# Kernel tuning notes

Hardware: AMD Instinct MI355X
Metric: run time of the kernel (lower is better)

The kernel has to match this reference:

```python
import jax, jax.numpy as jnp
import numpy as np

HEAD_DIM = 128
ALPHA0 = 1.0 / np.sqrt(HEAD_DIM).astype(np.float32)
ALPHA1 = 1.0


def setup_inputs() -> dict:
    key = jax.random.key(0)
    kq, kk, kv, kb = jax.random.split(key, 4)
    B, H, S, D = 2, 12, 2048, HEAD_DIM
    return {
        "q": jax.random.normal(kq, (B, H, S, D), dtype=jnp.float32),
        "k": jax.random.normal(kk, (B, H, S, D), dtype=jnp.float32),
        "v": jax.random.normal(kv, (B, H, S, D), dtype=jnp.float32),
        "bias": jax.random.normal(kb, (B, H, S, S), dtype=jnp.float32),
    }


def reference(q, k, v, bias):
    # output = alpha1 * sigmoid(alpha0 * (Q @ K^T) + bias) @ V
    scores = jnp.einsum("bhsd,bhtd->bhst", q, k)  # [B,H,S,S]
    attn = ALPHA1 * jax.nn.sigmoid(ALPHA0 * scores + bias)
    return jnp.einsum("bhst,bhtd->bhsd", attn, v)  # [B,H,S,D]
```

## Files before the change

### kernel.cpp

```cpp
#include <hip/hip_runtime.h>

typedef __attribute__((ext_vector_type(4))) float f32x4;
typedef __attribute__((ext_vector_type(8))) short short8v;
typedef __attribute__((ext_vector_type(2))) unsigned int uint2v;
typedef __attribute__((ext_vector_type(4))) unsigned int uint4v;

static constexpr int Sdim = 2048;
static constexpr int Ddim = 128;
static constexpr int BN   = 64;
static constexpr float kAlpha0 = 0.08838834764831844f;

__device__ __forceinline__ unsigned int bfpack(float a, float b) {
  unsigned int ua = __builtin_bit_cast(unsigned int, a);
  unsigned int ub = __builtin_bit_cast(unsigned int, b);
  ua = (ua + 0x7FFFu + ((ua >> 16) & 1u)) >> 16;
  ub = (ub + 0x7FFFu + ((ub >> 16) & 1u)) >> 16;
  return (ua & 0xFFFFu) | (ub << 16);
}

__device__ __forceinline__ float fast_sigmoid(float x) {
  return __builtin_amdgcn_rcpf(1.0f + __expf(-x));
}

__global__ __launch_bounds__(256, 2) void sigattn_kernel(
    const float* __restrict__ Q, const float* __restrict__ K,
    const float* __restrict__ V, const float* __restrict__ Bias,
    float* __restrict__ Out) {
  __shared__ __align__(16) unsigned char ldsK[BN * 256];
  __shared__ __align__(16) unsigned char ldsV[Ddim * 128];

  const int b    = blockIdx.x;
  const int xcd  = b & 7;
  const int jj   = b >> 3;
  const int head = xcd * 3 + (jj >> 4);
  const int q0   = (jj & 15) * 128;

  const int tid   = threadIdx.x;
  const int w     = tid >> 6;
  const int lane  = tid & 63;
  const int g     = lane >> 4;
  const int qlane = lane & 15;

  const float* __restrict__ Qh = Q + (size_t)head * Sdim * Ddim;
  const float* __restrict__ Kh = K + (size_t)head * Sdim * Ddim;
  const float* __restrict__ Vh = V + (size_t)head * Sdim * Ddim;
  const float* __restrict__ Bh = Bias + (size_t)head * Sdim * Sdim;
  float* __restrict__ Oh = Out + (size_t)head * Sdim * Ddim;

  short8v qfrag[2][4];
#pragma unroll
  for (int nf = 0; nf < 2; ++nf) {
    const float* qp = Qh + (size_t)(q0 + w * 32 + nf * 16 + qlane) * Ddim;
#pragma unroll
    for (int kf = 0; kf < 4; ++kf) {
      const int d0 = kf * 32 + g * 8;
      f32x4 a = *(const f32x4*)(qp + d0);
      f32x4 c = *(const f32x4*)(qp + d0 + 4);
      uint4v u;
      u[0] = bfpack(a[0], a[1]);
      u[1] = bfpack(a[2], a[3]);
      u[2] = bfpack(c[0], c[1]);
      u[3] = bfpack(c[2], c[3]);
      qfrag[nf][kf] = __builtin_bit_cast(short8v, u);
    }
  }

  const f32x4 fzero = {0.0f, 0.0f, 0.0f, 0.0f};
  f32x4 oacc[2][8];
#pragma unroll
  for (int qf = 0; qf < 2; ++qf)
#pragma unroll
    for (int nd = 0; nd < 8; ++nd) oacc[qf][nd] = fzero;

  const int idxA = ((((2 * g) & 3) * 16 + qlane) << 2);
  const int idxB = ((((2 * g + 1) & 3) * 16 + qlane) << 2);
  const bool lowhalf = (lane < 32);

  for (int t = 0; t < Sdim / BN; ++t) {
    const int kv0 = t * BN;

    {
      const int rb = tid >> 5;
      const int c4 = (tid & 31) * 4;
#pragma unroll
      for (int p = 0; p < 8; ++p) {
        const int r = p * 8 + rb;
        f32x4 kk = *(const f32x4*)(Kh + (size_t)(kv0 + r) * Ddim + c4);
        uint2v u;
        u[0] = bfpack(kk[0], kk[1]);
        u[1] = bfpack(kk[2], kk[3]);
        *(uint2v*)(ldsK + r * 256 + ((c4 * 2) ^ ((r & 7) << 4))) = u;
      }
    }
#pragma unroll
    for (int hh = 0; hh < 2; ++hh) {
      const int vb = tid + hh * 256;
      const int r0 = (vb >> 5) * 4;
      const int d4 = (vb & 31) * 4;
      f32x4 v0 = *(const f32x4*)(Vh + (size_t)(kv0 + r0 + 0) * Ddim + d4);
      f32x4 v1 = *(const f32x4*)(Vh + (size_t)(kv0 + r0 + 1) * Ddim + d4);
      f32x4 v2 = *(const f32x4*)(Vh + (size_t)(kv0 + r0 + 2) * Ddim + d4);
      f32x4 v3 = *(const f32x4*)(Vh + (size_t)(kv0 + r0 + 3) * Ddim + d4);
#pragma unroll
      for (int dd = 0; dd < 4; ++dd) {
        const int d = d4 + dd;
        uint2v u;
        u[0] = bfpack(v0[dd], v1[dd]);
        u[1] = bfpack(v2[dd], v3[dd]);
        *(uint2v*)(ldsV + d * 128 + ((r0 * 2) ^ (((d ^ (d >> 2)) & 7) << 4))) = u;
      }
    }
    __syncthreads();

    f32x4 bb[4][2];
#pragma unroll
    for (int mf = 0; mf < 4; ++mf)
#pragma unroll
      for (int nf = 0; nf < 2; ++nf) {
        const int row = q0 + w * 32 + nf * 16 + qlane;
        const int col = kv0 + mf * 16 + g * 4;
        bb[mf][nf] = *(const f32x4*)(Bh + (size_t)row * Sdim + col);
      }

    f32x4 sacc[4][2];
#pragma unroll
    for (int mf = 0; mf < 4; ++mf)
#pragma unroll
      for (int nf = 0; nf < 2; ++nf) sacc[mf][nf] = fzero;
#pragma unroll
    for (int kf = 0; kf < 4; ++kf)
#pragma unroll
      for (int mf = 0; mf < 4; ++mf) {
        const int kv = mf * 16 + qlane;
        const int d0 = kf * 32 + g * 8;
        short8v kf8 = *(const short8v*)(ldsK + kv * 256 + ((d0 * 2) ^ ((kv & 7) << 4)));
#pragma unroll
        for (int nf = 0; nf < 2; ++nf)
          sacc[mf][nf] = __builtin_amdgcn_mfma_f32_16x16x32_bf16(
              kf8, qfrag[nf][kf], sacc[mf][nf], 0, 0, 0);
      }

    unsigned int pw[4][2][2];
#pragma unroll
    for (int mf = 0; mf < 4; ++mf)
#pragma unroll
      for (int nf = 0; nf < 2; ++nf) {
        float p0 = fast_sigmoid(sacc[mf][nf][0] * kAlpha0 + bb[mf][nf][0]);
        float p1 = fast_sigmoid(sacc[mf][nf][1] * kAlpha0 + bb[mf][nf][1]);
        float p2 = fast_sigmoid(sacc[mf][nf][2] * kAlpha0 + bb[mf][nf][2]);
        float p3 = fast_sigmoid(sacc[mf][nf][3] * kAlpha0 + bb[mf][nf][3]);
        pw[mf][nf][0] = bfpack(p0, p1);
        pw[mf][nf][1] = bfpack(p2, p3);
      }

    short8v pa[2][2];
#pragma unroll
    for (int nf = 0; nf < 2; ++nf)
#pragma unroll
      for (int a = 0; a < 2; ++a) {
        uint4v u;
        int lo, hi;
        lo = __builtin_amdgcn_ds_bpermute(idxA, (int)pw[2 * a][nf][0]);
        hi = __builtin_amdgcn_ds_bpermute(idxA, (int)pw[2 * a + 1][nf][0]);
        u[0] = (unsigned)(lowhalf ? lo : hi);
        lo = __builtin_amdgcn_ds_bpermute(idxA, (int)pw[2 * a][nf][1]);
        hi = __builtin_amdgcn_ds_bpermute(idxA, (int)pw[2 * a + 1][nf][1]);
        u[1] = (unsigned)(lowhalf ? lo : hi);
        lo = __builtin_amdgcn_ds_bpermute(idxB, (int)pw[2 * a][nf][0]);
        hi = __builtin_amdgcn_ds_bpermute(idxB, (int)pw[2 * a + 1][nf][0]);
        u[2] = (unsigned)(lowhalf ? lo : hi);
        lo = __builtin_amdgcn_ds_bpermute(idxB, (int)pw[2 * a][nf][1]);
        hi = __builtin_amdgcn_ds_bpermute(idxB, (int)pw[2 * a + 1][nf][1]);
        u[3] = (unsigned)(lowhalf ? lo : hi);
        pa[nf][a] = __builtin_bit_cast(short8v, u);
      }

#pragma unroll
    for (int a = 0; a < 2; ++a)
#pragma unroll
      for (int nd = 0; nd < 8; ++nd) {
        const int d = nd * 16 + qlane;
        const int kvr = a * 32 + g * 8;
        short8v vf = *(const short8v*)(ldsV + d * 128 + ((kvr * 2) ^ (((d ^ (d >> 2)) & 7) << 4)));
#pragma unroll
        for (int qf = 0; qf < 2; ++qf)
          oacc[qf][nd] = __builtin_amdgcn_mfma_f32_16x16x32_bf16(
              pa[qf][a], vf, oacc[qf][nd], 0, 0, 0);
      }
    __syncthreads();
  }

#pragma unroll
  for (int qf = 0; qf < 2; ++qf)
#pragma unroll
    for (int nd = 0; nd < 8; ++nd) {
#pragma unroll
      for (int r = 0; r < 4; ++r) {
        const int row = q0 + w * 32 + qf * 16 + g * 4 + r;
        Oh[(size_t)row * Ddim + nd * 16 + qlane] = oacc[qf][nd][r];
      }
    }
}

extern "C" void kernel_launch(void* const* d_in, const int* in_sizes, int n_in,
                              void* d_out, int out_size, void* d_ws, size_t ws_size,
                              hipStream_t stream) {
  (void)in_sizes; (void)n_in; (void)d_ws; (void)ws_size; (void)out_size;
  const float* q    = (const float*)d_in[0];
  const float* k    = (const float*)d_in[1];
  const float* v    = (const float*)d_in[2];
  const float* bias = (const float*)d_in[3];
  float* out = (float*)d_out;
  dim3 grid(384), block(256);
  hipLaunchKernelGGL(sigattn_kernel, grid, block, 0, stream, q, k, v, bias, out);
}
```

Baseline: 632.3 us.

## Precompute bf16 K and transposed V, prefetch tiles via direct-to-LDS loads

```diff
diff --git a/kernel.cpp b/kernel.cpp
--- a/kernel.cpp
+++ b/kernel.cpp
@@ -2,12 +2,12 @@
 
 typedef __attribute__((ext_vector_type(4))) float f32x4;
 typedef __attribute__((ext_vector_type(8))) short short8v;
-typedef __attribute__((ext_vector_type(2))) unsigned int uint2v;
 typedef __attribute__((ext_vector_type(4))) unsigned int uint4v;
 
 static constexpr int Sdim = 2048;
 static constexpr int Ddim = 128;
 static constexpr int BN   = 64;
+static constexpr int NT   = Sdim / BN;
 static constexpr float kAlpha0 = 0.08838834764831844f;
 
 __device__ __forceinline__ unsigned int bfpack(float a, float b) {
@@ -17,23 +17,78 @@
   ub = (ub + 0x7FFFu + ((ub >> 16) & 1u)) >> 16;
   return (ua & 0xFFFFu) | (ub << 16);
 }
-
+__device__ __forceinline__ unsigned short bf1(float a) {
+  unsigned int ua = __builtin_bit_cast(unsigned int, a);
+  return (unsigned short)((ua + 0x7FFFu + ((ua >> 16) & 1u)) >> 16);
+}
 __device__ __forceinline__ float fast_sigmoid(float x) {
   return __builtin_amdgcn_rcpf(1.0f + __expf(-x));
 }
-
-__global__ __launch_bounds__(256, 2) void sigattn_kernel(
-    const float* __restrict__ Q, const float* __restrict__ K,
-    const float* __restrict__ V, const float* __restrict__ Bias,
+__device__ __forceinline__ void gll16(const void* g, void* l) {
+  __builtin_amdgcn_global_load_lds(
+      (const __attribute__((address_space(1))) unsigned int*)g,
+      (__attribute__((address_space(3))) unsigned int*)l, 16, 0, 0);
+}
+
+__global__ __launch_bounds__(256) void prep_kernel(
+    const float* __restrict__ K, const float* __restrict__ V,
+    unsigned short* __restrict__ Kb, unsigned short* __restrict__ Vt) {
+  __shared__ unsigned short ldsT[128 * 128];
+  const int head = blockIdx.x >> 4;
+  const int tile = blockIdx.x & 15;
+  const int t = threadIdx.x;
+  const float* Kh = K + ((size_t)head * Sdim + tile * 128) * Ddim;
+  const float* Vh = V + ((size_t)head * Sdim + tile * 128) * Ddim;
+  unsigned short* Kbh = Kb + ((size_t)head * Sdim + tile * 128) * Ddim;
+  unsigned short* Vth = Vt + (size_t)head * Ddim * Sdim + tile * 128;
+
+#pragma unroll
+  for (int c = 0; c < 8; ++c) {
+    const int e8 = c * 256 + t;
+    f32x4 a = *(const f32x4*)(Kh + e8 * 8);
+    f32x4 b = *(const f32x4*)(Kh + e8 * 8 + 4);
+    uint4v u;
+    u[0] = bfpack(a[0], a[1]); u[1] = bfpack(a[2], a[3]);
+    u[2] = bfpack(b[0], b[1]); u[3] = bfpack(b[2], b[3]);
+    *(uint4v*)(Kbh + e8 * 8) = u;
+  }
+#pragma unroll
+  for (int c = 0; c < 16; ++c) {
+    const int e4 = c * 256 + t;
+    const int kv = e4 >> 5;
+    const int c4 = (e4 & 31) * 4;
+    f32x4 v = *(const f32x4*)(Vh + (size_t)kv * Ddim + c4);
+#pragma unroll
+    for (int j = 0; j < 4; ++j) {
+      const int d = c4 + j;
+      const int sw = (d >> 2) & 7;
+      ldsT[d * 128 + ((((kv >> 3) ^ sw) << 3) | (kv & 7))] = bf1(v[j]);
+    }
+  }
+  __syncthreads();
+#pragma unroll
+  for (int c = 0; c < 8; ++c) {
+    const int G = c * 256 + t;
+    const int d = G >> 4;
+    const int s = G & 15;
+    const int sw = (d >> 2) & 7;
+    uint4v u = *(const uint4v*)(ldsT + d * 128 + ((s ^ sw) << 3));
+    *(uint4v*)(Vth + (size_t)d * Sdim + s * 8) = u;
+  }
+}
+
+__global__ __launch_bounds__(128, 2) void sigattn_kernel(
+    const float* __restrict__ Q, const unsigned short* __restrict__ Kb,
+    const unsigned short* __restrict__ Vt, const float* __restrict__ Bias,
     float* __restrict__ Out) {
-  __shared__ __align__(16) unsigned char ldsK[BN * 256];
-  __shared__ __align__(16) unsigned char ldsV[Ddim * 128];
+  __shared__ __align__(16) unsigned char lds[3 * 16384];
+  unsigned char* ldsK = lds;
 
   const int b    = blockIdx.x;
   const int xcd  = b & 7;
   const int jj   = b >> 3;
-  const int head = xcd * 3 + (jj >> 4);
-  const int q0   = (jj & 15) * 128;
+  const int head = xcd * 3 + (jj >> 5);
+  const int q0   = (jj & 31) * 64;
 
   const int tid   = threadIdx.x;
   const int w     = tid >> 6;
@@ -41,11 +96,28 @@
   const int g     = lane >> 4;
   const int qlane = lane & 15;
 
-  const float* __restrict__ Qh = Q + (size_t)head * Sdim * Ddim;
-  const float* __restrict__ Kh = K + (size_t)head * Sdim * Ddim;
-  const float* __restrict__ Vh = V + (size_t)head * Sdim * Ddim;
-  const float* __restrict__ Bh = Bias + (size_t)head * Sdim * Sdim;
-  float* __restrict__ Oh = Out + (size_t)head * Sdim * Ddim;
+  const float* Qh = Q + (size_t)head * Sdim * Ddim;
+  const unsigned short* KbH = Kb + (size_t)head * Sdim * Ddim;
+  const unsigned short* VtH = Vt + (size_t)head * Ddim * Sdim;
+  const float* Bh = Bias + (size_t)head * Sdim * Sdim;
+  float* Oh = Out + (size_t)head * Sdim * Ddim;
+
+  int koff[8], voff[8], dstb[8];
+#pragma unroll
+  for (int i = 0; i < 8; ++i) {
+    const int G = i * 128 + w * 64 + lane;
+    dstb[i] = (i * 128 + w * 64) * 16;
+    const int kv = G >> 4, s = G & 15;
+    koff[i] = kv * Ddim + ((s ^ (kv & 7)) << 3);
+    const int d = G >> 3, s2 = G & 7;
+    const int sw = (d ^ (d >> 2)) & 7;
+    voff[i] = d * Sdim + ((s2 ^ sw) << 3);
+  }
+
+#pragma unroll
+  for (int i = 0; i < 8; ++i) gll16(KbH + koff[i], ldsK + dstb[i]);
+#pragma unroll
+  for (int i = 0; i < 8; ++i) gll16(VtH + voff[i], lds + 16384 + dstb[i]);
 
   short8v qfrag[2][4];
 #pragma unroll
@@ -57,10 +129,8 @@
       f32x4 a = *(const f32x4*)(qp + d0);
       f32x4 c = *(const f32x4*)(qp + d0 + 4);
       uint4v u;
-      u[0] = bfpack(a[0], a[1]);
-      u[1] = bfpack(a[2], a[3]);
-      u[2] = bfpack(c[0], c[1]);
-      u[3] = bfpack(c[2], c[3]);
+      u[0] = bfpack(a[0], a[1]); u[1] = bfpack(a[2], a[3]);
+      u[2] = bfpack(c[0], c[1]); u[3] = bfpack(c[2], c[3]);
       qfrag[nf][kf] = __builtin_bit_cast(short8v, u);
     }
   }
@@ -76,40 +146,9 @@
   const int idxB = ((((2 * g + 1) & 3) * 16 + qlane) << 2);
   const bool lowhalf = (lane < 32);
 
-  for (int t = 0; t < Sdim / BN; ++t) {
+  int buf = 0;
+  for (int t = 0; t < NT; ++t) {
     const int kv0 = t * BN;
-
-    {
-      const int rb = tid >> 5;
-      const int c4 = (tid & 31) * 4;
-#pragma unroll
-      for (int p = 0; p < 8; ++p) {
-        const int r = p * 8 + rb;
-        f32x4 kk = *(const f32x4*)(Kh + (size_t)(kv0 + r) * Ddim + c4);
-        uint2v u;
-        u[0] = bfpack(kk[0], kk[1]);
-        u[1] = bfpack(kk[2], kk[3]);
-        *(uint2v*)(ldsK + r * 256 + ((c4 * 2) ^ ((r & 7) << 4))) = u;
-      }
-    }
-#pragma unroll
-    for (int hh = 0; hh < 2; ++hh) {
-      const int vb = tid + hh * 256;
-      const int r0 = (vb >> 5) * 4;
-      const int d4 = (vb & 31) * 4;
-      f32x4 v0 = *(const f32x4*)(Vh + (size_t)(kv0 + r0 + 0) * Ddim + d4);
-      f32x4 v1 = *(const f32x4*)(Vh + (size_t)(kv0 + r0 + 1) * Ddim + d4);
-      f32x4 v2 = *(const f32x4*)(Vh + (size_t)(kv0 + r0 + 2) * Ddim + d4);
-      f32x4 v3 = *(const f32x4*)(Vh + (size_t)(kv0 + r0 + 3) * Ddim + d4);
-#pragma unroll
-      for (int dd = 0; dd < 4; ++dd) {
-        const int d = d4 + dd;
-        uint2v u;
-        u[0] = bfpack(v0[dd], v1[dd]);
-        u[1] = bfpack(v2[dd], v3[dd]);
-        *(uint2v*)(ldsV + d * 128 + ((r0 * 2) ^ (((d ^ (d >> 2)) & 7) << 4))) = u;
-      }
-    }
     __syncthreads();
 
     f32x4 bb[4][2];
@@ -139,6 +178,19 @@
           sacc[mf][nf] = __builtin_amdgcn_mfma_f32_16x16x32_bf16(
               kf8, qfrag[nf][kf], sacc[mf][nf], 0, 0, 0);
       }
+
+    asm volatile("s_waitcnt lgkmcnt(0)" ::: "memory");
+    __builtin_amdgcn_s_barrier();
+    __builtin_amdgcn_sched_barrier(0);
+
+    if (t + 1 < NT) {
+      const int kvn = kv0 + BN;
+#pragma unroll
+      for (int i = 0; i < 8; ++i) gll16(KbH + kvn * Ddim + koff[i], ldsK + dstb[i]);
+      unsigned char* vb1 = lds + 16384 + (buf ^ 1) * 16384;
+#pragma unroll
+      for (int i = 0; i < 8; ++i) gll16(VtH + kvn + voff[i], vb1 + dstb[i]);
+    }
 
     unsigned int pw[4][2][2];
 #pragma unroll
@@ -175,42 +227,47 @@
         pa[nf][a] = __builtin_bit_cast(short8v, u);
       }
 
+    const unsigned char* vb = lds + 16384 + buf * 16384;
 #pragma unroll
     for (int a = 0; a < 2; ++a)
 #pragma unroll
       for (int nd = 0; nd < 8; ++nd) {
         const int d = nd * 16 + qlane;
         const int kvr = a * 32 + g * 8;
-        short8v vf = *(const short8v*)(ldsV + d * 128 + ((kvr * 2) ^ (((d ^ (d >> 2)) & 7) << 4)));
+        const int sw = (d ^ (d >> 2)) & 7;
+        short8v vf = *(const short8v*)(vb + d * 128 + ((kvr * 2) ^ (sw << 4)));
 #pragma unroll
         for (int qf = 0; qf < 2; ++qf)
           oacc[qf][nd] = __builtin_amdgcn_mfma_f32_16x16x32_bf16(
               pa[qf][a], vf, oacc[qf][nd], 0, 0, 0);
       }
-    __syncthreads();
+    buf ^= 1;
   }
 
 #pragma unroll
   for (int qf = 0; qf < 2; ++qf)
 #pragma unroll
-    for (int nd = 0; nd < 8; ++nd) {
+    for (int nd = 0; nd < 8; ++nd)
 #pragma unroll
       for (int r = 0; r < 4; ++r) {
         const int row = q0 + w * 32 + qf * 16 + g * 4 + r;
         Oh[(size_t)row * Ddim + nd * 16 + qlane] = oacc[qf][nd][r];
       }
-    }
 }
 
 extern "C" void kernel_launch(void* const* d_in, const int* in_sizes, int n_in,
                               void* d_out, int out_size, void* d_ws, size_t ws_size,
                               hipStream_t stream) {
-  (void)in_sizes; (void)n_in; (void)d_ws; (void)ws_size; (void)out_size;
+  (void)in_sizes; (void)n_in; (void)ws_size; (void)out_size;
   const float* q    = (const float*)d_in[0];
   const float* k    = (const float*)d_in[1];
   const float* v    = (const float*)d_in[2];
   const float* bias = (const float*)d_in[3];
   float* out = (float*)d_out;
-  dim3 grid(384), block(256);
-  hipLaunchKernelGGL(sigattn_kernel, grid, block, 0, stream, q, k, v, bias, out);
-}
+  unsigned short* Kb = (unsigned short*)d_ws;
+  unsigned short* Vt = Kb + (size_t)24 * Sdim * Ddim;
+
+  hipLaunchKernelGGL(prep_kernel, dim3(384), dim3(256), 0, stream, k, v, Kb, Vt);
+  hipLaunchKernelGGL(sigattn_kernel, dim3(768), dim3(128), 0, stream,
+                     q, Kb, Vt, bias, out);
+}
```

Result: no change. 630.5 us (-0.3%).
